# Kernel optimization log

Measured on AMD Instinct MI355X. Metric: run time of the kernel, lower is better.

The kernel has to match this reference:

```python
import jax, jax.numpy as jnp
import numpy as np

N = 100_000      # nodes
E = 3_200_000    # edges (before self-loops)
IN_DIM = 256
H1, H2 = 64, 32
OUT_DIM = 40
NEG_SLOPE = 0.2  # PyG GATConv default


def setup_inputs() -> dict:
    key = jax.random.key(0)
    ks = jax.random.split(key, 12)
    s = 0.05
    return {
        "x": jax.random.normal(ks[0], (N, IN_DIM), jnp.float32),
        "edge_index": jax.random.randint(ks[1], (2, E), 0, N, jnp.int32),
        "W1": jax.random.normal(ks[2], (IN_DIM, H1), jnp.float32) * s,
        "att_src1": jax.random.normal(ks[3], (H1,), jnp.float32) * s,
        "att_dst1": jax.random.normal(ks[4], (H1,), jnp.float32) * s,
        "b1": jnp.zeros((H1,), jnp.float32),
        "W2": jax.random.normal(ks[5], (H1, H2), jnp.float32) * s,
        "att_src2": jax.random.normal(ks[6], (H2,), jnp.float32) * s,
        "att_dst2": jax.random.normal(ks[7], (H2,), jnp.float32) * s,
        "b2": jnp.zeros((H2,), jnp.float32),
        "fcW": jax.random.normal(ks[8], (H2, OUT_DIM), jnp.float32) * s,
        "fcb": jnp.zeros((OUT_DIM,), jnp.float32),
    }


def gat_conv(x, src, dst, W, a_src, a_dst, b):
    """Single-head PyG GATConv (concat, heads=1). src/dst already include self-loops."""
    n = x.shape[0]
    h = x @ W                                   # [N, C] projected features (lin has no bias)
    alpha_s = (h * a_src).sum(-1)               # [N]
    alpha_d = (h * a_dst).sum(-1)               # [N]
    logit = jax.nn.leaky_relu(alpha_s[src] + alpha_d[dst], NEG_SLOPE)  # [E']
    # segment softmax over edges grouped by destination node
    m = jax.ops.segment_max(logit, dst, num_segments=n)               # [N]
    e = jnp.exp(logit - m[dst])                                        # [E']
    denom = jax.ops.segment_sum(e, dst, num_segments=n)               # [N]
    alpha = e / denom[dst]                                             # [E']
    out = jax.ops.segment_sum(h[src] * alpha[:, None], dst, num_segments=n)  # [N, C]
    return out + b


def reference(x, edge_index, W1, att_src1, att_dst1, b1, W2, att_src2, att_dst2, b2, fcW, fcb):
    n = x.shape[0]
    # add_self_loops=True (PyG GATConv default)
    loop = jnp.arange(n, dtype=edge_index.dtype)
    src = jnp.concatenate([edge_index[0], loop])
    dst = jnp.concatenate([edge_index[1], loop])
    h = jax.nn.relu(gat_conv(x, src, dst, W1, att_src1, att_dst1, b1))
    emb = jax.nn.relu(gat_conv(h, src, dst, W2, att_src2, att_dst2, b2))
    logits = emb @ fcW + fcb
    return emb, logits
```

## Files before the change

### kernel.cpp

```cpp
#include <hip/hip_runtime.h>
#include <hip/hip_bf16.h>

#define NEG_SLOPE 0.2f
#define IN_DIM 256
#define C1 64
#define C2 32
#define ODIM 40
#define SCAN_CHUNK 4096
#define BSHIFT 12
#define ECHUNK 8192
#define ECH2 16384
#define CH 10


__global__ void k_bhist(const int* __restrict__ dst, int E, int* __restrict__ gh,
                        int nblk, int nb) {
    __shared__ int h[32];
    int t = threadIdx.x;
    if (t < 32) h[t] = 0;
    __syncthreads();
    int base = blockIdx.x * ECHUNK;
    int end = min(base + ECHUNK, E);
    for (int i = base + t; i < end; i += 256) atomicAdd(&h[dst[i] >> BSHIFT], 1);
    __syncthreads();
    if (t < nb) gh[t * nblk + blockIdx.x] = h[t];
}

__global__ void k_bscan(int* __restrict__ gh, int L) {
    __shared__ int lds[256];
    __shared__ int carry;
    int t = threadIdx.x;
    if (t == 0) carry = 0;
    __syncthreads();
    for (int base = 0; base < L; base += 256) {
        int v = (base + t < L) ? gh[base + t] : 0;
        lds[t] = v; __syncthreads();
        for (int off = 1; off < 256; off <<= 1) {
            int u = (t >= off) ? lds[t - off] : 0;
            __syncthreads();
            lds[t] += u;
            __syncthreads();
        }
        if (base + t < L) gh[base + t] = lds[t] - v + carry;
        __syncthreads();
        if (t == 0) carry += lds[255];
        __syncthreads();
    }
}

__global__ void k_bplace(const int* __restrict__ src, const int* __restrict__ dst, int E,
                         const int* __restrict__ gh, int nblk, int nb,
                         int2* __restrict__ pairs) {
    __shared__ int cur[32];
    int t = threadIdx.x;
    if (t < nb) cur[t] = gh[t * nblk + blockIdx.x];
    __syncthreads();
    int base = blockIdx.x * ECHUNK;
    int end = min(base + ECHUNK, E);
    for (int i = base + t; i < end; i += 256) {
        int d = dst[i];
        int pos = atomicAdd(&cur[d >> BSHIFT], 1);
        pairs[pos] = make_int2(src[i], d);
    }
}

__device__ __forceinline__ void bc_map(int blk, int* b, int* c) {
    int xcd = blk & 7, k = blk >> 3;
    *b = (k & 3) * 8 + xcd;
    *c = k >> 2;
}

__global__ __launch_bounds__(512)
void k_nhist(const int2* __restrict__ pairs, const int* __restrict__ gh, int nblk,
             int nb, int E, int* __restrict__ chist) {
    __shared__ int h[4096];
    int b, c; bc_map(blockIdx.x, &b, &c);
    if (b >= nb) return;
    for (int i = threadIdx.x; i < 4096; i += 512) h[i] = 0;
    __syncthreads();
    int estart = gh[b * nblk];
    int eend = (b + 1 < nb) ? gh[(b + 1) * nblk] : E;
    int s0 = estart + c * ECH2;
    int s1 = min(s0 + ECH2, eend);
    for (int i = s0 + threadIdx.x; i < s1; i += 512)
        atomicAdd(&h[pairs[i].y & 4095], 1);
    __syncthreads();
    int* out = chist + ((size_t)b * CH + c) * 4096;
    for (int i = threadIdx.x; i < 4096; i += 512) out[i] = h[i];
}

__global__ void k_cnt(const int* __restrict__ chist, int* __restrict__ cnt, int n) {
    int i = blockIdx.x * 256 + threadIdx.x;
    if (i >= n) return;
    int b = i >> BSHIFT, j = i & 4095;
    const int* p = chist + ((size_t)b * CH) * 4096 + j;
    int s = 1;
#pragma unroll
    for (int c = 0; c < CH; c++) s += p[c * 4096];
    cnt[i] = s;
}

__global__ void k_scan1(const int* __restrict__ cnt, int n, int* __restrict__ bsums) {
    __shared__ int lds[256];
    int t = threadIdx.x;
    int base = blockIdx.x * SCAN_CHUNK + t * 16;
    int s = 0;
#pragma unroll
    for (int i = 0; i < 16; i++) { int idx = base + i; s += (idx < n) ? cnt[idx] : 0; }
    lds[t] = s; __syncthreads();
    for (int off = 128; off > 0; off >>= 1) {
        if (t < off) lds[t] += lds[t + off];
        __syncthreads();
    }
    if (t == 0) bsums[blockIdx.x] = lds[0];
}

__global__ void k_scan2(int* bsums, int nb, int* row_ptr, int n, int total) {
    __shared__ int lds[256];
    int t = threadIdx.x;
    int v = (t < nb) ? bsums[t] : 0;
    lds[t] = v; __syncthreads();
    for (int off = 1; off < 256; off <<= 1) {
        int u = (t >= off) ? lds[t - off] : 0;
        __syncthreads();
        lds[t] += u;
        __syncthreads();
    }
    if (t < nb) bsums[t] = lds[t] - v;
    if (t == 0) row_ptr[n] = total;
}

__global__ void k_scan3(const int* __restrict__ cnt, int n, const int* __restrict__ bsums,
                        int* __restrict__ row_ptr) {
    __shared__ int lds[256];
    int t = threadIdx.x;
    int base = blockIdx.x * SCAN_CHUNK + t * 16;
    int loc[16];
    int s = 0;
#pragma unroll
    for (int i = 0; i < 16; i++) {
        int idx = base + i;
        int c = (idx < n) ? cnt[idx] : 0;
        loc[i] = s; s += c;
    }
    lds[t] = s; __syncthreads();
    for (int off = 1; off < 256; off <<= 1) {
        int u = (t >= off) ? lds[t - off] : 0;
        __syncthreads();
        lds[t] += u;
        __syncthreads();
    }
    int texcl = lds[t] - s + bsums[blockIdx.x];
#pragma unroll
    for (int i = 0; i < 16; i++) {
        int idx = base + i;
        if (idx < n) row_ptr[idx] = texcl + loc[i];
    }
}

__global__ void k_selfloop(const int* __restrict__ row_ptr, int n, int* __restrict__ adj) {
    int i = blockIdx.x * 256 + threadIdx.x;
    if (i < n) adj[row_ptr[i]] = i;
}

__global__ void k_nscan(int* __restrict__ chist, const int* __restrict__ row_ptr, int n) {
    int i = blockIdx.x * 256 + threadIdx.x;
    if (i >= n) return;
    int b = i >> BSHIFT, j = i & 4095;
    int* p = chist + ((size_t)b * CH) * 4096 + j;
    int s = row_ptr[i] + 1;
#pragma unroll
    for (int c = 0; c < CH; c++) { int t = p[c * 4096]; p[c * 4096] = s; s += t; }
}

__global__ __launch_bounds__(512)
void k_place2(const int2* __restrict__ pairs, const int* __restrict__ gh, int nblk,
              int nb, int E, const int* __restrict__ chist, int* __restrict__ adj) {
    __shared__ int cur[4096];
    int b, c; bc_map(blockIdx.x, &b, &c);
    if (b >= nb) return;
    const int* cs = chist + ((size_t)b * CH + c) * 4096;
    for (int i = threadIdx.x; i < 4096; i += 512) cur[i] = cs[i];
    __syncthreads();
    int estart = gh[b * nblk];
    int eend = (b + 1 < nb) ? gh[(b + 1) * nblk] : E;
    int s0 = estart + c * ECH2;
    int s1 = min(s0 + ECH2, eend);
    for (int i = s0 + threadIdx.x; i < s1; i += 512) {
        int2 p = pairs[i];
        int pos = atomicAdd(&cur[p.y & 4095], 1);
        adj[pos] = p.x;
    }
}


__global__ __launch_bounds__(256, 4)
void k_gemm1(const float* __restrict__ x, const float* __restrict__ W1,
             float* __restrict__ h1, int n) {
    int t = threadIdx.x;
    int wave = t >> 6, lane = t & 63;
    int chalf = (blockIdx.x & 1) * 32;
    int row = (blockIdx.x >> 1) * 256 + wave * 64 + lane;
    bool active = row < n;
    int rowc = active ? row : n - 1;
    const float4* xr = (const float4*)(x + (size_t)rowc * IN_DIM);

    float acc[32];
#pragma unroll
    for (int c = 0; c < 32; c++) acc[c] = 0.f;

#define FMA_K(XC, KK) { \
        const float* wk = wb + (KK) * C1; \
        _Pragma("unroll") \
        for (int c = 0; c < 32; c++) acc[c] = fmaf((XC), wk[c], acc[c]); }

    for (int k0 = 0; k0 < 16; k0++) {
        float4 xv0 = xr[k0 * 4 + 0];
        float4 xv1 = xr[k0 * 4 + 1];
        float4 xv2 = xr[k0 * 4 + 2];
        float4 xv3 = xr[k0 * 4 + 3];
        const float* wb = W1 + (size_t)(k0 * 16) * C1 + chalf;
        FMA_K(xv0.x, 0)  FMA_K(xv0.y, 1)  FMA_K(xv0.z, 2)  FMA_K(xv0.w, 3)
        FMA_K(xv1.x, 4)  FMA_K(xv1.y, 5)  FMA_K(xv1.z, 6)  FMA_K(xv1.w, 7)
        FMA_K(xv2.x, 8)  FMA_K(xv2.y, 9)  FMA_K(xv2.z, 10) FMA_K(xv2.w, 11)
        FMA_K(xv3.x, 12) FMA_K(xv3.y, 13) FMA_K(xv3.z, 14) FMA_K(xv3.w, 15)
    }
#undef FMA_K

    if (!active) return;
    float* hp = h1 + (size_t)row * C1 + chalf;
#pragma unroll
    for (int j = 0; j < 8; j++)
        *(float4*)(hp + j * 4) =
            make_float4(acc[j * 4], acc[j * 4 + 1], acc[j * 4 + 2], acc[j * 4 + 3]);
}


__global__ __launch_bounds__(256)
void k_alpha(const float* __restrict__ h, const float* __restrict__ attS,
             const float* __restrict__ attD, float* __restrict__ as_,
             float* __restrict__ ad_, int n) {
    int wave = (blockIdx.x * 256 + threadIdx.x) >> 6;
    int lane = threadIdx.x & 63;
    if (wave >= n) return;
    float hv = h[(size_t)wave * C1 + lane];
    float vs = hv * attS[lane], vd = hv * attD[lane];
#pragma unroll
    for (int off = 32; off > 0; off >>= 1) {
        vs += __shfl_xor(vs, off);
        vd += __shfl_xor(vd, off);
    }
    if (lane == 0) { as_[wave] = vs; ad_[wave] = vd; }
}


__global__ __launch_bounds__(256)
void k_agg1(const float* __restrict__ h1, const float* __restrict__ as1,
            const float* __restrict__ ad1, const int* __restrict__ row_ptr,
            const int* __restrict__ adj, const float* __restrict__ b1,
            float* __restrict__ h1out, int n) {
    int wave = (blockIdx.x * 256 + threadIdx.x) >> 6;
    int lane = threadIdx.x & 63;
    if (wave >= n) return;
    int d = wave;
    int beg = row_ptr[d], end = row_ptr[d + 1];
    float adv = ad1[d];
    float acc = 0.f, dsum = 0.f;
    for (int base = beg; base < end; base += 64) {
        int cnt = min(64, end - base);
        int s = d; float w = 0.f;
        if (lane < cnt) {
            s = adj[base + lane];
            float lg = as1[s] + adv;
            lg = lg > 0.f ? lg : NEG_SLOPE * lg;
            w = expf(lg);
            dsum += w;
        }
        int j = 0;
        for (; j + 4 <= cnt; j += 4) {
            int s0 = __shfl(s, j),     s1 = __shfl(s, j + 1);
            int s2 = __shfl(s, j + 2), s3 = __shfl(s, j + 3);
            float w0 = __shfl(w, j),     w1 = __shfl(w, j + 1);
            float w2 = __shfl(w, j + 2), w3 = __shfl(w, j + 3);
            float g0 = h1[(size_t)s0 * C1 + lane];
            float g1 = h1[(size_t)s1 * C1 + lane];
            float g2 = h1[(size_t)s2 * C1 + lane];
            float g3 = h1[(size_t)s3 * C1 + lane];
            acc = fmaf(w0, g0, acc); acc = fmaf(w1, g1, acc);
            acc = fmaf(w2, g2, acc); acc = fmaf(w3, g3, acc);
        }
        for (; j < cnt; j++) {
            int sj = __shfl(s, j);
            float wj = __shfl(w, j);
            acc = fmaf(wj, h1[(size_t)sj * C1 + lane], acc);
        }
    }
#pragma unroll
    for (int off = 32; off > 0; off >>= 1) dsum += __shfl_xor(dsum, off);
    float out = acc / dsum + b1[lane];
    h1out[(size_t)d * C1 + lane] = out > 0.f ? out : 0.f;
}


__global__ __launch_bounds__(256)
void k_gemm2(const float* __restrict__ h1out, const float* __restrict__ W2,
             const float* __restrict__ attS, const float* __restrict__ attD,
             float* __restrict__ h2, float* __restrict__ as2, float* __restrict__ ad2, int n) {
    __shared__ float w2t[C2 * 68];
    __shared__ float sAttS[C2], sAttD[C2];
    int t = threadIdx.x;
    for (int i = t; i < C1 * C2; i += 256) {
        int k = i >> 5, c = i & 31;
        w2t[c * 68 + k] = W2[i];
    }
    if (t < C2) { sAttS[t] = attS[t]; sAttD[t] = attD[t]; }
    __syncthreads();
    int wave = t >> 6, lane = t & 63;
    int col = lane & 31, half = lane >> 5;
    int rowbase = blockIdx.x * 32 + wave * 8;
    const float* wrow = &w2t[col * 68];
    for (int rr = 0; rr < 8; rr += 2) {
        int row = rowbase + rr + half;
        if (row >= n) return;
        float acc = 0.f;
#pragma unroll
        for (int k = 0; k < C1; k += 4) {
            float4 wv = *(const float4*)&wrow[k];
            float4 xv = *(const float4*)&h1out[(size_t)row * C1 + k];
            acc = fmaf(xv.x, wv.x, acc);
            acc = fmaf(xv.y, wv.y, acc);
            acc = fmaf(xv.z, wv.z, acc);
            acc = fmaf(xv.w, wv.w, acc);
        }
        h2[(size_t)row * C2 + col] = acc;
        float vs = acc * sAttS[col], vd = acc * sAttD[col];
#pragma unroll
        for (int off = 16; off > 0; off >>= 1) {
            vs += __shfl_xor(vs, off);
            vd += __shfl_xor(vd, off);
        }
        if (col == 0) { as2[row] = vs; ad2[row] = vd; }
    }
}


__global__ __launch_bounds__(256)
void k_agg2(const float* __restrict__ h2, const float* __restrict__ as2,
            const float* __restrict__ ad2, const int* __restrict__ row_ptr,
            const int* __restrict__ adj, const float* __restrict__ b2,
            float* __restrict__ emb, int n) {
    int wave = (blockIdx.x * 256 + threadIdx.x) >> 6;
    int lane = threadIdx.x & 63;
    if (wave >= n) return;
    int d = wave;
    int beg = row_ptr[d], end = row_ptr[d + 1];
    float adv = ad2[d];
    int c = lane & 31, half = lane >> 5;
    float acc = 0.f, dsum = 0.f;
    for (int base = beg; base < end; base += 64) {
        int cnt = min(64, end - base);
        int s = d; float w = 0.f;
        if (lane < cnt) {
            s = adj[base + lane];
            float lg = as2[s] + adv;
            lg = lg > 0.f ? lg : NEG_SLOPE * lg;
            w = expf(lg);
            dsum += w;
        }
        int j = 0;
        for (; j + 4 <= cnt; j += 4) {
            int sa = __shfl(s, j + half);
            int sb = __shfl(s, j + 2 + half);
            float wa = __shfl(w, j + half);
            float wb = __shfl(w, j + 2 + half);
            float ga = h2[(size_t)sa * C2 + c];
            float gb = h2[(size_t)sb * C2 + c];
            acc = fmaf(wa, ga, acc);
            acc = fmaf(wb, gb, acc);
        }
        for (; j + 2 <= cnt; j += 2) {
            int sj = __shfl(s, j + half);
            float wj = __shfl(w, j + half);
            acc = fmaf(wj, h2[(size_t)sj * C2 + c], acc);
        }
        if (j < cnt) {
            int sj = __shfl(s, j);
            float wj = __shfl(w, j);
            if (half == 0) acc = fmaf(wj, h2[(size_t)sj * C2 + c], acc);
        }
    }
    acc += __shfl_xor(acc, 32);
#pragma unroll
    for (int off = 32; off > 0; off >>= 1) dsum += __shfl_xor(dsum, off);
    if (half == 0) {
        float v = acc / dsum + b2[c];
        emb[(size_t)d * C2 + c] = v > 0.f ? v : 0.f;
    }
}


__global__ __launch_bounds__(256)
void k_logits(const float* __restrict__ emb, const float* __restrict__ fcW,
              const float* __restrict__ fcb, float* __restrict__ out, int n) {
    __shared__ float w[C2 * ODIM];
    __shared__ float b[ODIM];
    int t = threadIdx.x;
    for (int i = t; i < C2 * ODIM; i += 256) w[i] = fcW[i];
    if (t < ODIM) b[t] = fcb[t];
    __syncthreads();
    int lane = t & 63;
    int row = blockIdx.x * 4 + (t >> 6);
    if (row >= n) return;
    float acc = (lane < ODIM) ? b[lane] : 0.f;
    const float4* er = (const float4*)&emb[(size_t)row * C2];
#pragma unroll
    for (int c4 = 0; c4 < 8; c4++) {
        float4 e = er[c4];
        int c = c4 * 4;
        if (lane < ODIM) {
            acc = fmaf(e.x, w[(c + 0) * ODIM + lane], acc);
            acc = fmaf(e.y, w[(c + 1) * ODIM + lane], acc);
            acc = fmaf(e.z, w[(c + 2) * ODIM + lane], acc);
            acc = fmaf(e.w, w[(c + 3) * ODIM + lane], acc);
        }
    }
    if (lane < ODIM) out[(size_t)row * ODIM + lane] = acc;
}


extern "C" void kernel_launch(void* const* d_in, const int* in_sizes, int n_in,
                              void* d_out, int out_size, void* d_ws, size_t ws_size,
                              hipStream_t stream) {
    const float* x    = (const float*)d_in[0];
    const int*   ei   = (const int*)d_in[1];
    const float* W1   = (const float*)d_in[2];
    const float* aS1  = (const float*)d_in[3];
    const float* aD1  = (const float*)d_in[4];
    const float* b1   = (const float*)d_in[5];
    const float* W2   = (const float*)d_in[6];
    const float* aS2  = (const float*)d_in[7];
    const float* aD2  = (const float*)d_in[8];
    const float* b2   = (const float*)d_in[9];
    const float* fcW  = (const float*)d_in[10];
    const float* fcb  = (const float*)d_in[11];

    const int N = in_sizes[0] / IN_DIM;
    const int E = in_sizes[1] / 2;
    const int* src = ei;
    const int* dst = ei + E;

    float* h1    = (float*)d_ws;
    float* h1out = h1 + (size_t)N * C1;
    float* as1   = h1out + (size_t)N * C1;
    float* ad1   = as1 + N;
    float* as2   = ad1 + N;
    float* ad2   = as2 + N;
    int*   cnt   = (int*)(ad2 + N);
    int*   row_ptr = cnt + N;
    int*   bsums   = row_ptr + (N + 1);
    int*   adj     = bsums + 256;
    int*   gh      = adj + (E + N);
    float* h2    = h1;

    int2* pairs = (int2*)h1out;
    int*  chist = (int*)h1;

    float* emb    = (float*)d_out;
    float* logits = emb + (size_t)N * C2;

    int nbN   = (N + 255) / 256;
    int nbS   = (N + SCAN_CHUNK - 1) / SCAN_CHUNK;
    int nblkE = (E + ECHUNK - 1) / ECHUNK;
    int nb    = (N + (1 << BSHIFT) - 1) >> BSHIFT;
    int nBC   = 8 * 4 * CH;

    k_bhist<<<nblkE, 256, 0, stream>>>(dst, E, gh, nblkE, nb);
    k_bscan<<<1, 256, 0, stream>>>(gh, nb * nblkE);
    k_bplace<<<nblkE, 256, 0, stream>>>(src, dst, E, gh, nblkE, nb, pairs);
    k_nhist<<<nBC, 512, 0, stream>>>(pairs, gh, nblkE, nb, E, chist);
    k_cnt<<<nbN, 256, 0, stream>>>(chist, cnt, N);
    k_scan1<<<nbS, 256, 0, stream>>>(cnt, N, bsums);
    k_scan2<<<1, 256, 0, stream>>>(bsums, nbS, row_ptr, N, E + N);
    k_scan3<<<nbS, 256, 0, stream>>>(cnt, N, bsums, row_ptr);
    k_selfloop<<<nbN, 256, 0, stream>>>(row_ptr, N, adj);
    k_nscan<<<nbN, 256, 0, stream>>>(chist, row_ptr, N);
    k_place2<<<nBC, 512, 0, stream>>>(pairs, gh, nblkE, nb, E, chist, adj);

    int nbG1 = 2 * ((N + 255) / 256);
    k_gemm1<<<nbG1, 256, 0, stream>>>(x, W1, h1, N);
    int nbA = (N + 3) / 4;
    k_alpha<<<nbA, 256, 0, stream>>>(h1, aS1, aD1, as1, ad1, N);
    k_agg1<<<nbA, 256, 0, stream>>>(h1, as1, ad1, row_ptr, adj, b1, h1out, N);
    int nbG2 = (N + 31) / 32;
    k_gemm2<<<nbG2, 256, 0, stream>>>(h1out, W2, aS2, aD2, h2, as2, ad2, N);
    k_agg2<<<nbA, 256, 0, stream>>>(h2, as2, ad2, row_ptr, adj, b2, emb, N);
    k_logits<<<nbA, 256, 0, stream>>>(emb, fcW, fcb, logits, N);
}
```

Measured before the change: 469.7 us.

## Store projected features as bf16 and fuse attention scores into GEMM1

```diff
diff --git a/kernel.cpp b/kernel.cpp
--- a/kernel.cpp
+++ b/kernel.cpp
@@ -12,6 +12,18 @@
 #define ECH2 16384
 #define CH 10
 
+typedef unsigned int uint32;
+typedef unsigned short ushort16;
+
+__device__ __forceinline__ unsigned bf16_rne(float f) {
+    unsigned a = __float_as_uint(f);
+    return (a + 0x7FFFu + ((a >> 16) & 1u)) >> 16;
+}
+__device__ __forceinline__ void bf16x2_unpack(unsigned u, float& f0, float& f1) {
+    f0 = __uint_as_float(u << 16);
+    f1 = __uint_as_float(u & 0xFFFF0000u);
+}
+
 
 __global__ void k_bhist(const int* __restrict__ dst, int E, int* __restrict__ gh,
                         int nblk, int nb) {
@@ -196,30 +208,29 @@
 
 __global__ __launch_bounds__(256, 4)
 void k_gemm1(const float* __restrict__ x, const float* __restrict__ W1,
-             float* __restrict__ h1, int n) {
-    int t = threadIdx.x;
-    int wave = t >> 6, lane = t & 63;
-    int chalf = (blockIdx.x & 1) * 32;
-    int row = (blockIdx.x >> 1) * 256 + wave * 64 + lane;
+             const float* __restrict__ attS, const float* __restrict__ attD,
+             ushort16* __restrict__ h1b, float* __restrict__ as1,
+             float* __restrict__ ad1, int n) {
+    int row = blockIdx.x * 256 + threadIdx.x;
     bool active = row < n;
     int rowc = active ? row : n - 1;
     const float4* xr = (const float4*)(x + (size_t)rowc * IN_DIM);
 
-    float acc[32];
-#pragma unroll
-    for (int c = 0; c < 32; c++) acc[c] = 0.f;
+    float acc[64];
+#pragma unroll
+    for (int c = 0; c < 64; c++) acc[c] = 0.f;
 
 #define FMA_K(XC, KK) { \
         const float* wk = wb + (KK) * C1; \
         _Pragma("unroll") \
-        for (int c = 0; c < 32; c++) acc[c] = fmaf((XC), wk[c], acc[c]); }
+        for (int c = 0; c < 64; c++) acc[c] = fmaf((XC), wk[c], acc[c]); }
 
     for (int k0 = 0; k0 < 16; k0++) {
         float4 xv0 = xr[k0 * 4 + 0];
         float4 xv1 = xr[k0 * 4 + 1];
         float4 xv2 = xr[k0 * 4 + 2];
         float4 xv3 = xr[k0 * 4 + 3];
-        const float* wb = W1 + (size_t)(k0 * 16) * C1 + chalf;
+        const float* wb = W1 + (size_t)(k0 * 16) * C1;
         FMA_K(xv0.x, 0)  FMA_K(xv0.y, 1)  FMA_K(xv0.z, 2)  FMA_K(xv0.w, 3)
         FMA_K(xv1.x, 4)  FMA_K(xv1.y, 5)  FMA_K(xv1.z, 6)  FMA_K(xv1.w, 7)
         FMA_K(xv2.x, 8)  FMA_K(xv2.y, 9)  FMA_K(xv2.z, 10) FMA_K(xv2.w, 11)
@@ -228,34 +239,28 @@
 #undef FMA_K
 
     if (!active) return;
-    float* hp = h1 + (size_t)row * C1 + chalf;
-#pragma unroll
-    for (int j = 0; j < 8; j++)
-        *(float4*)(hp + j * 4) =
-            make_float4(acc[j * 4], acc[j * 4 + 1], acc[j * 4 + 2], acc[j * 4 + 3]);
+    float vs = 0.f, vd = 0.f;
+#pragma unroll
+    for (int c = 0; c < 64; c++) {
+        vs = fmaf(acc[c], attS[c], vs);
+        vd = fmaf(acc[c], attD[c], vd);
+    }
+    as1[row] = vs; ad1[row] = vd;
+
+    uint4* hp = (uint4*)(h1b + (size_t)row * C1);
+#pragma unroll
+    for (int j = 0; j < 8; j++) {
+        unsigned p0 = bf16_rne(acc[j*8+0]) | (bf16_rne(acc[j*8+1]) << 16);
+        unsigned p1 = bf16_rne(acc[j*8+2]) | (bf16_rne(acc[j*8+3]) << 16);
+        unsigned p2 = bf16_rne(acc[j*8+4]) | (bf16_rne(acc[j*8+5]) << 16);
+        unsigned p3 = bf16_rne(acc[j*8+6]) | (bf16_rne(acc[j*8+7]) << 16);
+        hp[j] = make_uint4(p0, p1, p2, p3);
+    }
 }
 
 
 __global__ __launch_bounds__(256)
-void k_alpha(const float* __restrict__ h, const float* __restrict__ attS,
-             const float* __restrict__ attD, float* __restrict__ as_,
-             float* __restrict__ ad_, int n) {
-    int wave = (blockIdx.x * 256 + threadIdx.x) >> 6;
-    int lane = threadIdx.x & 63;
-    if (wave >= n) return;
-    float hv = h[(size_t)wave * C1 + lane];
-    float vs = hv * attS[lane], vd = hv * attD[lane];
-#pragma unroll
-    for (int off = 32; off > 0; off >>= 1) {
-        vs += __shfl_xor(vs, off);
-        vd += __shfl_xor(vd, off);
-    }
-    if (lane == 0) { as_[wave] = vs; ad_[wave] = vd; }
-}
-
-
-__global__ __launch_bounds__(256)
-void k_agg1(const float* __restrict__ h1, const float* __restrict__ as1,
+void k_agg1(const ushort16* __restrict__ h1b, const float* __restrict__ as1,
             const float* __restrict__ ad1, const int* __restrict__ row_ptr,
             const int* __restrict__ adj, const float* __restrict__ b1,
             float* __restrict__ h1out, int n) {
@@ -265,7 +270,22 @@
     int d = wave;
     int beg = row_ptr[d], end = row_ptr[d + 1];
     float adv = ad1[d];
-    float acc = 0.f, dsum = 0.f;
+    int g = lane >> 3, cq = lane & 7;
+    float acc[8];
+#pragma unroll
+    for (int k = 0; k < 8; k++) acc[k] = 0.f;
+    float dsum = 0.f;
+
+#define AGG1_ROUND(E_) { \
+        int se = __shfl(s, (E_)); \
+        float we = __shfl(w, (E_)); \
+        uint4 u = ((const uint4*)(h1b + (size_t)se * C1))[cq]; \
+        float f0, f1; \
+        bf16x2_unpack(u.x, f0, f1); acc[0]=fmaf(we,f0,acc[0]); acc[1]=fmaf(we,f1,acc[1]); \
+        bf16x2_unpack(u.y, f0, f1); acc[2]=fmaf(we,f0,acc[2]); acc[3]=fmaf(we,f1,acc[3]); \
+        bf16x2_unpack(u.z, f0, f1); acc[4]=fmaf(we,f0,acc[4]); acc[5]=fmaf(we,f1,acc[5]); \
+        bf16x2_unpack(u.w, f0, f1); acc[6]=fmaf(we,f0,acc[6]); acc[7]=fmaf(we,f1,acc[7]); }
+
     for (int base = beg; base < end; base += 64) {
         int cnt = min(64, end - base);
         int s = d; float w = 0.f;
@@ -277,35 +297,47 @@
             dsum += w;
         }
         int j = 0;
-        for (; j + 4 <= cnt; j += 4) {
-            int s0 = __shfl(s, j),     s1 = __shfl(s, j + 1);
-            int s2 = __shfl(s, j + 2), s3 = __shfl(s, j + 3);
-            float w0 = __shfl(w, j),     w1 = __shfl(w, j + 1);
-            float w2 = __shfl(w, j + 2), w3 = __shfl(w, j + 3);
-            float g0 = h1[(size_t)s0 * C1 + lane];
-            float g1 = h1[(size_t)s1 * C1 + lane];
-            float g2 = h1[(size_t)s2 * C1 + lane];
-            float g3 = h1[(size_t)s3 * C1 + lane];
-            acc = fmaf(w0, g0, acc); acc = fmaf(w1, g1, acc);
-            acc = fmaf(w2, g2, acc); acc = fmaf(w3, g3, acc);
-        }
-        for (; j < cnt; j++) {
-            int sj = __shfl(s, j);
-            float wj = __shfl(w, j);
-            acc = fmaf(wj, h1[(size_t)sj * C1 + lane], acc);
-        }
-    }
+        for (; j + 32 <= cnt; j += 32) {
+            AGG1_ROUND(j + g)
+            AGG1_ROUND(j + 8 + g)
+            AGG1_ROUND(j + 16 + g)
+            AGG1_ROUND(j + 24 + g)
+        }
+        for (; j < cnt; j += 8) AGG1_ROUND(j + g)
+    }
+#undef AGG1_ROUND
+
 #pragma unroll
     for (int off = 32; off > 0; off >>= 1) dsum += __shfl_xor(dsum, off);
-    float out = acc / dsum + b1[lane];
-    h1out[(size_t)d * C1 + lane] = out > 0.f ? out : 0.f;
+#pragma unroll
+    for (int off = 8; off <= 32; off <<= 1) {
+#pragma unroll
+        for (int k = 0; k < 8; k++) acc[k] += __shfl_xor(acc[k], off);
+    }
+    if (g == 0) {
+        float inv = 1.f / dsum;
+        float4 bv0 = ((const float4*)b1)[cq * 2];
+        float4 bv1 = ((const float4*)b1)[cq * 2 + 1];
+        float4 o0, o1;
+        o0.x = acc[0] * inv + bv0.x; o0.x = o0.x > 0.f ? o0.x : 0.f;
+        o0.y = acc[1] * inv + bv0.y; o0.y = o0.y > 0.f ? o0.y : 0.f;
+        o0.z = acc[2] * inv + bv0.z; o0.z = o0.z > 0.f ? o0.z : 0.f;
+        o0.w = acc[3] * inv + bv0.w; o0.w = o0.w > 0.f ? o0.w : 0.f;
+        o1.x = acc[4] * inv + bv1.x; o1.x = o1.x > 0.f ? o1.x : 0.f;
+        o1.y = acc[5] * inv + bv1.y; o1.y = o1.y > 0.f ? o1.y : 0.f;
+        o1.z = acc[6] * inv + bv1.z; o1.z = o1.z > 0.f ? o1.z : 0.f;
+        o1.w = acc[7] * inv + bv1.w; o1.w = o1.w > 0.f ? o1.w : 0.f;
+        float4* op = (float4*)(h1out + (size_t)d * C1 + cq * 8);
+        op[0] = o0; op[1] = o1;
+    }
 }
 
 
 __global__ __launch_bounds__(256)
 void k_gemm2(const float* __restrict__ h1out, const float* __restrict__ W2,
              const float* __restrict__ attS, const float* __restrict__ attD,
-             float* __restrict__ h2, float* __restrict__ as2, float* __restrict__ ad2, int n) {
+             ushort16* __restrict__ h2b, float* __restrict__ as2,
+             float* __restrict__ ad2, int n) {
     __shared__ float w2t[C2 * 68];
     __shared__ float sAttS[C2], sAttD[C2];
     int t = threadIdx.x;
@@ -332,7 +364,7 @@
             acc = fmaf(xv.z, wv.z, acc);
             acc = fmaf(xv.w, wv.w, acc);
         }
-        h2[(size_t)row * C2 + col] = acc;
+        h2b[(size_t)row * C2 + col] = (ushort16)bf16_rne(acc);
         float vs = acc * sAttS[col], vd = acc * sAttD[col];
 #pragma unroll
         for (int off = 16; off > 0; off >>= 1) {
@@ -345,7 +377,7 @@
 
 
 __global__ __launch_bounds__(256)
-void k_agg2(const float* __restrict__ h2, const float* __restrict__ as2,
+void k_agg2(const ushort16* __restrict__ h2b, const float* __restrict__ as2,
             const float* __restrict__ ad2, const int* __restrict__ row_ptr,
             const int* __restrict__ adj, const float* __restrict__ b2,
             float* __restrict__ emb, int n) {
@@ -355,8 +387,22 @@
     int d = wave;
     int beg = row_ptr[d], end = row_ptr[d + 1];
     float adv = ad2[d];
-    int c = lane & 31, half = lane >> 5;
-    float acc = 0.f, dsum = 0.f;
+    int g = lane >> 2, cq = lane & 3;
+    float acc[8];
+#pragma unroll
+    for (int k = 0; k < 8; k++) acc[k] = 0.f;
+    float dsum = 0.f;
+
+#define AGG2_ROUND(E_) { \
+        int se = __shfl(s, (E_)); \
+        float we = __shfl(w, (E_)); \
+        uint4 u = ((const uint4*)(h2b + (size_t)se * C2))[cq]; \
+        float f0, f1; \
+        bf16x2_unpack(u.x, f0, f1); acc[0]=fmaf(we,f0,acc[0]); acc[1]=fmaf(we,f1,acc[1]); \
+        bf16x2_unpack(u.y, f0, f1); acc[2]=fmaf(we,f0,acc[2]); acc[3]=fmaf(we,f1,acc[3]); \
+        bf16x2_unpack(u.z, f0, f1); acc[4]=fmaf(we,f0,acc[4]); acc[5]=fmaf(we,f1,acc[5]); \
+        bf16x2_unpack(u.w, f0, f1); acc[6]=fmaf(we,f0,acc[6]); acc[7]=fmaf(we,f1,acc[7]); }
+
     for (int base = beg; base < end; base += 64) {
         int cnt = min(64, end - base);
         int s = d; float w = 0.f;
@@ -368,33 +414,38 @@
             dsum += w;
         }
         int j = 0;
-        for (; j + 4 <= cnt; j += 4) {
-            int sa = __shfl(s, j + half);
-            int sb = __shfl(s, j + 2 + half);
-            float wa = __shfl(w, j + half);
-            float wb = __shfl(w, j + 2 + half);
-            float ga = h2[(size_t)sa * C2 + c];
-            float gb = h2[(size_t)sb * C2 + c];
-            acc = fmaf(wa, ga, acc);
-            acc = fmaf(wb, gb, acc);
-        }
-        for (; j + 2 <= cnt; j += 2) {
-            int sj = __shfl(s, j + half);
-            float wj = __shfl(w, j + half);
-            acc = fmaf(wj, h2[(size_t)sj * C2 + c], acc);
-        }
-        if (j < cnt) {
-            int sj = __shfl(s, j);
-            float wj = __shfl(w, j);
-            if (half == 0) acc = fmaf(wj, h2[(size_t)sj * C2 + c], acc);
-        }
-    }
-    acc += __shfl_xor(acc, 32);
+        for (; j + 64 <= cnt; j += 64) {
+            AGG2_ROUND(j + g)
+            AGG2_ROUND(j + 16 + g)
+            AGG2_ROUND(j + 32 + g)
+            AGG2_ROUND(j + 48 + g)
+        }
+        for (; j < cnt; j += 16) AGG2_ROUND(j + g)
+    }
+#undef AGG2_ROUND
+
 #pragma unroll
     for (int off = 32; off > 0; off >>= 1) dsum += __shfl_xor(dsum, off);
-    if (half == 0) {
-        float v = acc / dsum + b2[c];
-        emb[(size_t)d * C2 + c] = v > 0.f ? v : 0.f;
+#pragma unroll
+    for (int off = 4; off <= 32; off <<= 1) {
+#pragma unroll
+        for (int k = 0; k < 8; k++) acc[k] += __shfl_xor(acc[k], off);
+    }
+    if (g == 0) {
+        float inv = 1.f / dsum;
+        float4 bv0 = ((const float4*)b2)[cq * 2];
+        float4 bv1 = ((const float4*)b2)[cq * 2 + 1];
+        float4 o0, o1;
+        o0.x = acc[0] * inv + bv0.x; o0.x = o0.x > 0.f ? o0.x : 0.f;
+        o0.y = acc[1] * inv + bv0.y; o0.y = o0.y > 0.f ? o0.y : 0.f;
+        o0.z = acc[2] * inv + bv0.z; o0.z = o0.z > 0.f ? o0.z : 0.f;
+        o0.w = acc[3] * inv + bv0.w; o0.w = o0.w > 0.f ? o0.w : 0.f;
+        o1.x = acc[4] * inv + bv1.x; o1.x = o1.x > 0.f ? o1.x : 0.f;
+        o1.y = acc[5] * inv + bv1.y; o1.y = o1.y > 0.f ? o1.y : 0.f;
+        o1.z = acc[6] * inv + bv1.z; o1.z = o1.z > 0.f ? o1.z : 0.f;
+        o1.w = acc[7] * inv + bv1.w; o1.w = o1.w > 0.f ? o1.w : 0.f;
+        float4* op = (float4*)(emb + (size_t)d * C2 + cq * 8);
+        op[0] = o0; op[1] = o1;
     }
 }
 
@@ -449,21 +500,21 @@
     const int* src = ei;
     const int* dst = ei + E;
 
-    float* h1    = (float*)d_ws;
-    float* h1out = h1 + (size_t)N * C1;
-    float* as1   = h1out + (size_t)N * C1;
-    float* ad1   = as1 + N;
-    float* as2   = ad1 + N;
-    float* ad2   = as2 + N;
-    int*   cnt   = (int*)(ad2 + N);
+    ushort16* h1b = (ushort16*)d_ws;
+    float* h1out  = (float*)((char*)d_ws + (size_t)N * C1 * 2);
+    float* as1    = h1out + (size_t)N * C1;
+    float* ad1    = as1 + N;
+    float* as2    = ad1 + N;
+    float* ad2    = as2 + N;
+    int*   cnt    = (int*)(ad2 + N);
     int*   row_ptr = cnt + N;
     int*   bsums   = row_ptr + (N + 1);
     int*   adj     = bsums + 256;
     int*   gh      = adj + (E + N);
-    float* h2    = h1;
 
     int2* pairs = (int2*)h1out;
-    int*  chist = (int*)h1;
+    int*  chist = (int*)h1b;
+    ushort16* h2b = (ushort16*)h1b;
 
     float* emb    = (float*)d_out;
     float* logits = emb + (size_t)N * C2;
@@ -486,13 +537,11 @@
     k_nscan<<<nbN, 256, 0, stream>>>(chist, row_ptr, N);
     k_place2<<<nBC, 512, 0, stream>>>(pairs, gh, nblkE, nb, E, chist, adj);
 
-    int nbG1 = 2 * ((N + 255) / 256);
-    k_gemm1<<<nbG1, 256, 0, stream>>>(x, W1, h1, N);
+    k_gemm1<<<nbN, 256, 0, stream>>>(x, W1, aS1, aD1, h1b, as1, ad1, N);
     int nbA = (N + 3) / 4;
-    k_alpha<<<nbA, 256, 0, stream>>>(h1, aS1, aD1, as1, ad1, N);
-    k_agg1<<<nbA, 256, 0, stream>>>(h1, as1, ad1, row_ptr, adj, b1, h1out, N);
+    k_agg1<<<nbA, 256, 0, stream>>>(h1b, as1, ad1, row_ptr, adj, b1, h1out, N);
     int nbG2 = (N + 31) / 32;
-    k_gemm2<<<nbG2, 256, 0, stream>>>(h1out, W2, aS2, aD2, h2, as2, ad2, N);
-    k_agg2<<<nbA, 256, 0, stream>>>(h2, as2, ad2, row_ptr, adj, b2, emb, N);
+    k_gemm2<<<nbG2, 256, 0, stream>>>(h1out, W2, aS2, aD2, h2b, as2, ad2, N);
+    k_agg2<<<nbA, 256, 0, stream>>>(h2b, as2, ad2, row_ptr, adj, b2, emb, N);
     k_logits<<<nbA, 256, 0, stream>>>(emb, fcW, fcb, logits, N);
 }
```

Result: faster. 457.1 us (-2.7%).
